# Kernel optimization log

Measured on AMD Instinct MI355X. Metric: run time of the kernel, lower is better.

Reference implementation:

```python
import jax, jax.numpy as jnp
import numpy as np

H = 128; ED = 16; NF = 200000; EI = 800000; NT = 20000; M = 4; NM = NT * M; EG = 320000; NHEADS = 4


def _ln(x, g, b):
    mu = x.mean(-1, keepdims=True)
    v = ((x - mu) ** 2).mean(-1, keepdims=True)
    return (x - mu) / jnp.sqrt(v + 1e-5) * g + b


def _bn(x, g, b):
    mu = x.mean(0)
    v = ((x - mu) ** 2).mean(0)
    return (x - mu) / jnp.sqrt(v + 1e-5) * g + b


def _gine(x, ei, ea, We, be, W1, b1, W2, b2):
    # GINEConv: msg = relu(x_j + Lin(e_ji)), sum-aggr, eps=0, 2-layer MLP
    msg = jax.nn.relu(x[ei[0]] + ea @ We.T + be)
    agg = jax.ops.segment_sum(msg, ei[1], num_segments=x.shape[0])
    z = x + agg
    return jax.nn.relu(z @ W1.T + b1) @ W2.T + b2


def _view_attn(x, ln1_g, ln1_b, ln2_g, ln2_b, Wqkv, bqkv, Wo, bo, fW1, fb1, fW2, fb2):
    N, m, Hd = x.shape
    dh = Hd // NHEADS
    r = _ln(x, ln1_g, ln1_b)
    qkv = r @ Wqkv.T + bqkv
    q, k, v = jnp.split(qkv, 3, axis=-1)
    q = q.reshape(N, m, NHEADS, dh)
    k = k.reshape(N, m, NHEADS, dh)
    v = v.reshape(N, m, NHEADS, dh)
    s = jnp.einsum('nqhd,nkhd->nhqk', q, k) * (dh ** -0.5)
    a = jax.nn.softmax(s, axis=-1)
    o = jnp.einsum('nhqk,nkhd->nqhd', a, v).reshape(N, m, Hd)
    x = x + o @ Wo.T + bo
    y = _ln(x, ln2_g, ln2_b)
    x = x + jax.nn.gelu(y @ fW1.T + fb1, approximate=False) @ fW2.T + fb2
    return x.mean(axis=1)


def setup_inputs() -> dict:
    key = jax.random.key(0)
    ks = jax.random.split(key, 48)
    rn = lambda i, shape, s=0.02: jax.random.normal(ks[i], shape, jnp.float32) * s
    inp = {}
    inp['h_flat'] = jax.random.normal(ks[0], (NF, H), jnp.float32)
    inp['ea_flat'] = jax.random.normal(ks[1], (EI, ED), jnp.float32)
    inp['edge_attr'] = jax.random.normal(ks[2], (EG, ED), jnp.float32)
    inp['intra_ei'] = jax.random.randint(ks[3], (2, EI), 0, NF)
    inp['edge_index'] = jax.random.randint(ks[4], (2, EG), 0, NT)
    inp['node_ids'] = jax.random.randint(ks[5], (NF,), 0, NT)
    inp['sub_batch'] = jax.random.randint(ks[6], (NF,), 0, NM)
    inp['root_flat_idx'] = jax.random.randint(ks[7], (NM,), 0, NF)
    inp['valid'] = jnp.ones((NF,), jnp.bool_)
    inp['N_total'] = NT
    inp['m'] = M
    inp['Wskip'] = rn(8, (H, H)); inp['bskip'] = jnp.zeros((H,))
    inp['Wvv'] = rn(9, (H, H)); inp['bvv'] = jnp.zeros((H,))
    inp['Wkk'] = rn(10, (H, H)); inp['bkk'] = jnp.zeros((H,))
    inp['lc_We'] = rn(11, (H, ED)); inp['lc_be'] = jnp.zeros((H,))
    inp['lc_W1'] = rn(12, (H, H)); inp['lc_b1'] = jnp.zeros((H,))
    inp['lc_W2'] = rn(13, (H, H)); inp['lc_b2'] = jnp.zeros((H,))
    inp['gc_We'] = rn(14, (H, ED)); inp['gc_be'] = jnp.zeros((H,))
    inp['gc_W1'] = rn(15, (H, H)); inp['gc_b1'] = jnp.zeros((H,))
    inp['gc_W2'] = rn(16, (H, H)); inp['gc_b2'] = jnp.zeros((H,))
    inp['lbn_g'] = jnp.ones((H,)); inp['lbn_b'] = jnp.zeros((H,))
    inp['gbn_g'] = jnp.ones((H,)); inp['gbn_b'] = jnp.zeros((H,))
    inp['ln1_g'] = jnp.ones((H,)); inp['ln1_b'] = jnp.zeros((H,))
    inp['ln2_g'] = jnp.ones((H,)); inp['ln2_b'] = jnp.zeros((H,))
    inp['Wqkv'] = rn(17, (3 * H, H)); inp['bqkv'] = jnp.zeros((3 * H,))
    inp['Wo'] = rn(18, (H, H)); inp['bo'] = jnp.zeros((H,))
    inp['ffn_W1'] = rn(19, (4 * H, H)); inp['ffn_b1'] = jnp.zeros((4 * H,))
    inp['ffn_W2'] = rn(20, (H, 4 * H)); inp['ffn_b2'] = jnp.zeros((H,))
    return inp


def reference(h_flat, ea_flat, edge_attr, intra_ei, edge_index, node_ids, sub_batch,
              root_flat_idx, valid, N_total, m,
              Wskip, bskip, Wvv, bvv, Wkk, bkk,
              lc_We, lc_be, lc_W1, lc_b1, lc_W2, lc_b2,
              gc_We, gc_be, gc_W1, gc_b1, gc_W2, gc_b2,
              lbn_g, lbn_b, gbn_g, gbn_b,
              ln1_g, ln1_b, ln2_g, ln2_b,
              Wqkv, bqkv, Wo, bo, ffn_W1, ffn_b1, ffn_W2, ffn_b2):
    valid_f = valid.astype(jnp.float32)[:, None]                      # [NF,1]
    clamped = jnp.maximum(node_ids, 0)
    valid_mask = (node_ids >= 0).astype(jnp.float32)[:, None]
    h_skip = (h_flat @ Wskip.T + bskip) * valid_f
    h1 = _gine(h_flat, intra_ei, ea_flat, lc_We, lc_be, lc_W1, lc_b1, lc_W2, lc_b2)
    h1 = _bn(h1, lbn_g, lbn_b) * valid_f
    # scatter-mean of valid rows into N_total global nodes
    sums = jax.ops.segment_sum(h_flat * valid_mask, clamped, num_segments=N_total)
    cnt = jax.ops.segment_sum(valid_mask, clamped, num_segments=N_total)
    x_sum = sums / jnp.maximum(cnt, 1.0)
    h_global = _gine(x_sum, edge_index, edge_attr, gc_We, gc_be, gc_W1, gc_b1, gc_W2, gc_b2)
    h2 = _bn(h_global, gbn_g, gbn_b)[clamped] * valid_f
    h_roots3d = h_flat[root_flat_idx].reshape(N_total, m, H)
    x_vv_node = _view_attn(h_roots3d, ln1_g, ln1_b, ln2_g, ln2_b, Wqkv, bqkv, Wo, bo,
                           ffn_W1, ffn_b1, ffn_W2, ffn_b2)
    x_vv = (x_vv_node[clamped] @ Wvv.T + bvv) * valid_f
    x_kk = (h_flat[root_flat_idx[sub_batch]] @ Wkk.T + bkk) * valid_f
    out = jax.nn.relu(h_skip + h1 + h2 + x_vv + x_kk)
    return out * valid_f
```

## Files before the change

### kernel.cpp

```cpp
#include <hip/hip_runtime.h>
#include <math.h>

typedef __bf16 bf16_t;
typedef bf16_t bf16x8 __attribute__((ext_vector_type(8)));
typedef float  f32x4  __attribute__((ext_vector_type(4)));

#define DEV static __device__ __forceinline__

constexpr int H  = 128, ED = 16;
constexpr int NF = 200000, EI = 800000, NT = 20000, MV = 4, NM = NT*MV, EG = 320000;

DEV bf16x8 ldb8(const bf16_t* p){ union{uint4 u; bf16x8 v;} t; t.u = *(const uint4*)p; return t.v; }
DEV void   stb8(bf16_t* p, bf16x8 v){ union{uint4 u; bf16x8 f;} t; t.f=v; *(uint4*)p = t.u; }

DEV bf16x8 cvt8(const float* p){
  float4 a = *(const float4*)p, b = *(const float4*)(p+4);
  bf16x8 r;
  r[0]=(bf16_t)a.x; r[1]=(bf16_t)a.y; r[2]=(bf16_t)a.z; r[3]=(bf16_t)a.w;
  r[4]=(bf16_t)b.x; r[5]=(bf16_t)b.y; r[6]=(bf16_t)b.z; r[7]=(bf16_t)b.w;
  return r;
}
DEV bf16x8 cvtadd8(const float* p, const float* q){
  float4 a = *(const float4*)p, b = *(const float4*)(p+4);
  float4 c = *(const float4*)q, d = *(const float4*)(q+4);
  bf16x8 r;
  r[0]=(bf16_t)(a.x+c.x); r[1]=(bf16_t)(a.y+c.y); r[2]=(bf16_t)(a.z+c.z); r[3]=(bf16_t)(a.w+c.w);
  r[4]=(bf16_t)(b.x+d.x); r[5]=(bf16_t)(b.y+d.y); r[6]=(bf16_t)(b.z+d.z); r[7]=(bf16_t)(b.w+d.w);
  return r;
}

struct GArgs {
  const float*  A;      const bf16_t* Abf;   const float* Aadd;  const int* gidx;
  const float*  W;      const float*  bias;
  float*        outf;   bf16_t*       outb;
  const float*  Xadd_f; const bf16_t* Xadd_b; const int* gidx2;
  const bf16_t* B1;     const bf16_t* h2pre; const float* yvv;  const bf16_t* ykk;
  const int*    node_ids; const int*  sub_batch; const float* affine;
  int nrows; int ldout;
};

constexpr int A_F32=0, A_F32_ADD=1, A_BF16=2, A_F32_GATHER=3;
constexpr int E_BIAS_BF16=0, E_RELU_BF16=1, E_GELU_BF16=2, E_BIAS_F32=3,
              E_ADDGATHER_BF16=4, E_ADDROW_BF16=5, E_FINAL=6;

template<int AM>
DEV bf16x8 loadA(const GArgs& g, int row, int koff, int K){
  if constexpr (AM==A_BF16)        return ldb8(g.Abf + (size_t)row*K + koff);
  else if constexpr (AM==A_F32)    return cvt8(g.A   + (size_t)row*K + koff);
  else if constexpr (AM==A_F32_GATHER) return cvt8(g.A + (size_t)g.gidx[row]*K + koff);
  else { size_t o = (size_t)row*K + koff; return cvtadd8(g.A + o, g.Aadd + o); }
}

template<int K, int CTPW, int AM, int EPI>
__global__ __launch_bounds__(256) void k_gemm(GArgs g){
  constexpr int NS = K/32;
  const int lane = threadIdx.x & 63;
  const int wave = threadIdx.x >> 6;
  const int quad = lane >> 4;
  const int r16  = lane & 15;
  const int colBase = (blockIdx.y*4 + wave)*(CTPW*16);

  bf16x8 bfrag[CTPW][NS];
  float  bcol[CTPW];
  #pragma unroll
  for (int c=0;c<CTPW;c++){
    const float* wrow = g.W + (size_t)(colBase + c*16 + r16)*K;
    #pragma unroll
    for (int s=0;s<NS;s++) bfrag[c][s] = cvt8(wrow + s*32 + quad*8);
    bcol[c] = g.bias[colBase + c*16 + r16];
  }
  float aLc[CTPW], bLc[CTPW], aGc[CTPW], bGc[CTPW];
  if constexpr (EPI==E_FINAL){
    #pragma unroll
    for (int c=0;c<CTPW;c++){
      int col = colBase + c*16 + r16;
      aLc[c]=g.affine[col];     bLc[c]=g.affine[128+col];
      aGc[c]=g.affine[256+col]; bGc[c]=g.affine[384+col];
    }
  }

  const int row0 = blockIdx.x*64;
  #pragma unroll 1
  for (int t=0;t<4;t++){
    int rowbase = row0 + t*16;
    if (rowbase >= g.nrows) break;
    int arow = rowbase + r16;
    f32x4 acc[CTPW] = {};
    #pragma unroll
    for (int s=0;s<NS;s++){
      bf16x8 af = loadA<AM>(g, arow, s*32 + quad*8, K);
      #pragma unroll
      for (int c=0;c<CTPW;c++)
        acc[c] = __builtin_amdgcn_mfma_f32_16x16x32_bf16(af, bfrag[c][s], acc[c], 0, 0, 0);
    }
    #pragma unroll
    for (int r=0;r<4;r++){
      int orow = rowbase + quad*4 + r;
      int nid=0, sb=0, g2=0;
      if constexpr (EPI==E_FINAL){ nid = g.node_ids[orow]; sb = g.sub_batch[orow]; }
      if constexpr (EPI==E_ADDGATHER_BF16){ g2 = g.gidx2[orow]; }
      #pragma unroll
      for (int c=0;c<CTPW;c++){
        int col = colBase + c*16 + r16;
        float v = acc[c][r] + bcol[c];
        size_t oidx = (size_t)orow*g.ldout + col;
        if constexpr (EPI==E_BIAS_BF16)      g.outb[oidx] = (bf16_t)v;
        else if constexpr (EPI==E_RELU_BF16) g.outb[oidx] = (bf16_t)fmaxf(v,0.f);
        else if constexpr (EPI==E_GELU_BF16){
          float gv = 0.5f*v*(1.f + erff(v*0.70710678118654752f));
          g.outb[oidx] = (bf16_t)gv;
        }
        else if constexpr (EPI==E_BIAS_F32)  g.outf[oidx] = v;
        else if constexpr (EPI==E_ADDGATHER_BF16){
          v += g.Xadd_f[(size_t)g2*128 + col];
          g.outb[oidx] = (bf16_t)v;
        }
        else if constexpr (EPI==E_ADDROW_BF16){
          v += (float)g.Xadd_b[(size_t)orow*128 + col];
          g.outb[oidx] = (bf16_t)v;
        }
        else if constexpr (EPI==E_FINAL){
          v += (float)g.ykk[(size_t)sb*128 + col];
          v += g.yvv[(size_t)nid*128 + col];
          v += (float)g.B1[(size_t)orow*128 + col]*aLc[c] + bLc[c];
          v += (float)g.h2pre[(size_t)nid*128 + col]*aGc[c] + bGc[c];
          g.outf[oidx] = fmaxf(v, 0.f);
        }
      }
    }
  }
}

template<int CHUNK>
__global__ __launch_bounds__(256) void k_edge(const float* x, const float* ea, const int* ei,
                                              const float* We, const float* be, float* agg, int E){
  __shared__ float eaL[CHUNK*16];
  __shared__ int   srcL[CHUNK], dstL[CHUNK];
  const int c = threadIdx.x & 127, half = threadIdx.x >> 7;
  float w[16];
  #pragma unroll
  for (int d=0;d<16;d++) w[d] = We[c*16+d];
  const float bc = be[c];
  const int e0 = blockIdx.x * CHUNK;
  for (int i=threadIdx.x; i<CHUNK*16; i+=256) eaL[i] = ea[(size_t)e0*16 + i];
  for (int i=threadIdx.x; i<CHUNK;    i+=256){ srcL[i]=ei[e0+i]; dstL[i]=ei[(size_t)E+e0+i]; }
  __syncthreads();
  for (int i=half; i<CHUNK; i+=2){
    const float4* ep = (const float4*)(eaL + i*16);
    float4 e1=ep[0], e2=ep[1], e3=ep[2], e4=ep[3];
    float p = bc;
    p += e1.x*w[0] + e1.y*w[1] + e1.z*w[2] + e1.w*w[3];
    p += e2.x*w[4] + e2.y*w[5] + e2.z*w[6] + e2.w*w[7];
    p += e3.x*w[8] + e3.y*w[9] + e3.z*w[10]+ e3.w*w[11];
    p += e4.x*w[12]+ e4.y*w[13]+ e4.z*w[14]+ e4.w*w[15];
    float msg = fmaxf(x[(size_t)srcL[i]*128 + c] + p, 0.f);
    atomicAdd(agg + (size_t)dstL[i]*128 + c, msg);
  }
}

__global__ __launch_bounds__(256) void k_smean(const float* h, const int* nid, float* xs, float* cnt){
  int gid = blockIdx.x*256 + threadIdx.x;
  int i = gid >> 5;
  if (i >= NF) return;
  int q = gid & 31;
  int t = nid[i];
  float4 v = *(const float4*)(h + (size_t)i*128 + q*4);
  float* d = xs + (size_t)t*128 + q*4;
  atomicAdd(d+0, v.x); atomicAdd(d+1, v.y); atomicAdd(d+2, v.z); atomicAdd(d+3, v.w);
  if (q==0) atomicAdd(cnt + t, 1.f);
}

__global__ __launch_bounds__(256) void k_div(float* xs, const float* cnt){
  int gid = blockIdx.x*256 + threadIdx.x;
  int n = gid >> 5;
  if (n >= NT) return;
  int q = gid & 31;
  float inv = 1.f / fmaxf(cnt[n], 1.f);
  float4* p = (float4*)(xs + (size_t)n*128 + q*4);
  float4 v = *p;
  v.x*=inv; v.y*=inv; v.z*=inv; v.w*=inv;
  *p = v;
}

__global__ __launch_bounds__(256) void k_stats(const bf16_t* X, int nrows, float* stats){
  int c = threadIdx.x & 127, ro = threadIdx.x >> 7;
  int r0 = blockIdx.x*256;
  int rend = (r0+256 < nrows) ? r0+256 : nrows;
  float s1=0.f, s2=0.f;
  for (int i=r0+ro; i<rend; i+=2){
    float v = (float)X[(size_t)i*128 + c];
    s1 += v; s2 += v*v;
  }
  atomicAdd(stats + c,       s1);
  atomicAdd(stats + 128 + c, s2);
}

__global__ void k_affine(const float* sL, const float* sG,
                         const float* lg, const float* lb, const float* gg, const float* gb,
                         float nL, float nG, float* aff){
  int c = threadIdx.x;
  float muL = sL[c]/nL, vL = sL[128+c]/nL - muL*muL;
  float aL = lg[c]*rsqrtf(vL + 1e-5f);
  aff[c] = aL; aff[128+c] = lb[c] - muL*aL;
  float muG = sG[c]/nG, vG = sG[128+c]/nG - muG*muG;
  float aG = gg[c]*rsqrtf(vG + 1e-5f);
  aff[256+c] = aG; aff[384+c] = gb[c] - muG*aG;
}

template<int MODE>
__global__ __launch_bounds__(256) void k_ln(const float* Xf, const bf16_t* Xb, const int* gidx,
                                            const float* gamma, const float* beta, bf16_t* outp, int nrows){
  int wave = threadIdx.x >> 6, lane = threadIdx.x & 63;
  int row = blockIdx.x*4 + wave;
  if (row >= nrows) return;
  int c0 = lane*2;
  float x0, x1;
  if constexpr (MODE==0){
    const float* p = Xf + (size_t)gidx[row]*128;
    x0 = p[c0]; x1 = p[c0+1];
  } else {
    const bf16_t* p = Xb + (size_t)row*128;
    x0 = (float)p[c0]; x1 = (float)p[c0+1];
  }
  float s = x0 + x1, q = x0*x0 + x1*x1;
  #pragma unroll
  for (int m=1; m<64; m<<=1){ s += __shfl_xor(s, m); q += __shfl_xor(q, m); }
  float mu = s*(1.f/128.f);
  float var = q*(1.f/128.f) - mu*mu;
  float rs = rsqrtf(var + 1e-5f);
  outp[(size_t)row*128 + c0]   = (bf16_t)((x0-mu)*rs*gamma[c0]   + beta[c0]);
  outp[(size_t)row*128 + c0+1] = (bf16_t)((x1-mu)*rs*gamma[c0+1] + beta[c0+1]);
}

__global__ __launch_bounds__(256) void k_attn(const bf16_t* qkv, bf16_t* o, int nnodes){
  int wave = threadIdx.x >> 6, lane = threadIdx.x & 63;
  int node = blockIdx.x*4 + wave;
  if (node >= nnodes) return;
  int qv = lane >> 4, hh = (lane >> 2) & 3, sub = lane & 3;
  size_t base = (size_t)node*4*384;
  int coff = hh*32 + sub*8;
  bf16x8 qf = ldb8(qkv + base + (size_t)qv*384 + coff);
  float s[4];
  #pragma unroll
  for (int kv=0;kv<4;kv++){
    bf16x8 kf = ldb8(qkv + base + (size_t)kv*384 + 128 + coff);
    float p = 0.f;
    #pragma unroll
    for (int j=0;j<8;j++) p += (float)qf[j]*(float)kf[j];
    p += __shfl_xor(p, 1);
    p += __shfl_xor(p, 2);
    s[kv] = p * 0.17677669529663687f;
  }
  float mx = fmaxf(fmaxf(s[0],s[1]), fmaxf(s[2],s[3]));
  float e[4]; float sm = 0.f;
  #pragma unroll
  for (int kv=0;kv<4;kv++){ e[kv] = expf(s[kv]-mx); sm += e[kv]; }
  float inv = 1.f/sm;
  float ov[8] = {0,0,0,0,0,0,0,0};
  #pragma unroll
  for (int kv=0;kv<4;kv++){
    float a = e[kv]*inv;
    bf16x8 vf = ldb8(qkv + base + (size_t)kv*384 + 256 + coff);
    #pragma unroll
    for (int j=0;j<8;j++) ov[j] += a*(float)vf[j];
  }
  bf16x8 of;
  #pragma unroll
  for (int j=0;j<8;j++) of[j] = (bf16_t)ov[j];
  stb8(o + (size_t)(node*4+qv)*128 + coff, of);
}

__global__ __launch_bounds__(256) void k_mean(const bf16_t* z2, bf16_t* xvvn){
  int gid = blockIdx.x*256 + threadIdx.x;
  if (gid >= NT*128) return;
  int n = gid >> 7, c = gid & 127;
  size_t b = (size_t)n*4*128 + c;
  float v = (float)z2[b] + (float)z2[b+128] + (float)z2[b+256] + (float)z2[b+384];
  xvvn[(size_t)n*128 + c] = (bf16_t)(v*0.25f);
}

extern "C" void kernel_launch(void* const* d_in, const int* in_sizes, int n_in,
                              void* d_out, int out_size, void* d_ws, size_t ws_size,
                              hipStream_t stream)
{
  const float* h_flat    = (const float*)d_in[0];
  const float* ea_flat   = (const float*)d_in[1];
  const float* edge_attr = (const float*)d_in[2];
  const int*   intra_ei  = (const int*)d_in[3];
  const int*   edge_index= (const int*)d_in[4];
  const int*   node_ids  = (const int*)d_in[5];
  const int*   sub_batch = (const int*)d_in[6];
  const int*   root_idx  = (const int*)d_in[7];
  const float* Wskip = (const float*)d_in[11]; const float* bskip = (const float*)d_in[12];
  const float* Wvv   = (const float*)d_in[13]; const float* bvv   = (const float*)d_in[14];
  const float* Wkk   = (const float*)d_in[15]; const float* bkk   = (const float*)d_in[16];
  const float* lc_We = (const float*)d_in[17]; const float* lc_be = (const float*)d_in[18];
  const float* lc_W1 = (const float*)d_in[19]; const float* lc_b1 = (const float*)d_in[20];
  const float* lc_W2 = (const float*)d_in[21]; const float* lc_b2 = (const float*)d_in[22];
  const float* gc_We = (const float*)d_in[23]; const float* gc_be = (const float*)d_in[24];
  const float* gc_W1 = (const float*)d_in[25]; const float* gc_b1 = (const float*)d_in[26];
  const float* gc_W2 = (const float*)d_in[27]; const float* gc_b2 = (const float*)d_in[28];
  const float* lbn_g = (const float*)d_in[29]; const float* lbn_b = (const float*)d_in[30];
  const float* gbn_g = (const float*)d_in[31]; const float* gbn_b = (const float*)d_in[32];
  const float* ln1_g = (const float*)d_in[33]; const float* ln1_b = (const float*)d_in[34];
  const float* ln2_g = (const float*)d_in[35]; const float* ln2_b = (const float*)d_in[36];
  const float* Wqkv  = (const float*)d_in[37]; const float* bqkv  = (const float*)d_in[38];
  const float* Wo    = (const float*)d_in[39]; const float* bo    = (const float*)d_in[40];
  const float* fW1   = (const float*)d_in[41]; const float* fb1   = (const float*)d_in[42];
  const float* fW2   = (const float*)d_in[43]; const float* fb2   = (const float*)d_in[44];
  float* out = (float*)d_out;

  char* base = (char*)d_ws;
  size_t off = 0;
  auto carve = [&](size_t bytes)->char* {
    char* p = base + off; off += (bytes + 255) & ~(size_t)255; return p;
  };
  float*  agg   = (float*) carve((size_t)NF*H*4);
  bf16_t* qkv   = (bf16_t*)agg;
  bf16_t* tbuf  = (bf16_t*)carve((size_t)NM*512*2);
  bf16_t* mid   = tbuf;
  bf16_t* B1    = (bf16_t*)carve((size_t)NF*H*2);
  bf16_t* rbuf  = (bf16_t*)carve((size_t)NM*H*2);
  bf16_t* z2    = rbuf;
  bf16_t* obuf  = (bf16_t*)carve((size_t)NM*H*2);
  bf16_t* xattn = (bf16_t*)carve((size_t)NM*H*2);
  bf16_t* ykk   = xattn;
  bf16_t* ybuf  = (bf16_t*)carve((size_t)NM*H*2);
  float*  x_sum = (float*) carve((size_t)NT*H*4);
  float*  yvv   = x_sum;
  float*  aggG  = (float*) carve((size_t)NT*H*4);
  float*  cnt   = (float*) carve((size_t)NT*4);
  bf16_t* tG    = (bf16_t*)carve((size_t)NT*H*2);
  bf16_t* h2pre = (bf16_t*)carve((size_t)NT*H*2);
  bf16_t* xvvn  = (bf16_t*)carve((size_t)NT*H*2);
  float*  statsL= (float*) carve(256*4);
  float*  statsG= (float*) carve(256*4);
  float*  affine= (float*) carve(512*4);
  if (off > ws_size) return;

  hipMemsetAsync(agg,    0, (size_t)NF*H*4, stream);
  hipMemsetAsync(x_sum,  0, (size_t)NT*H*4, stream);
  hipMemsetAsync(aggG,   0, (size_t)NT*H*4, stream);
  hipMemsetAsync(cnt,    0, (size_t)NT*4,   stream);
  hipMemsetAsync(statsL, 0, 2048,           stream);

  auto GX = [](int n){ return (unsigned)((n + 63) / 64); };

  k_edge<64><<<EI/64, 256, 0, stream>>>(h_flat, ea_flat, intra_ei, lc_We, lc_be, agg, EI);
  k_smean<<<(NF*32)/256, 256, 0, stream>>>(h_flat, node_ids, x_sum, cnt);
  k_div<<<(NT*32)/256, 256, 0, stream>>>(x_sum, cnt);
  k_edge<64><<<EG/64, 256, 0, stream>>>(x_sum, edge_attr, edge_index, gc_We, gc_be, aggG, EG);
  { GArgs a{}; a.A=x_sum; a.Aadd=aggG; a.W=gc_W1; a.bias=gc_b1; a.outb=tG; a.nrows=NT; a.ldout=H;
    k_gemm<128,2,A_F32_ADD,E_RELU_BF16><<<dim3(GX(NT),1), 256, 0, stream>>>(a); }
  { GArgs a{}; a.Abf=tG; a.W=gc_W2; a.bias=gc_b2; a.outb=h2pre; a.nrows=NT; a.ldout=H;
    k_gemm<128,2,A_BF16,E_BIAS_BF16><<<dim3(GX(NT),1), 256, 0, stream>>>(a); }
  k_stats<<<(NT+255)/256, 256, 0, stream>>>(h2pre, NT, statsG);
  { GArgs a{}; a.A=h_flat; a.Aadd=agg; a.W=lc_W1; a.bias=lc_b1; a.outb=tbuf; a.nrows=NF; a.ldout=H;
    k_gemm<128,2,A_F32_ADD,E_RELU_BF16><<<dim3(GX(NF),1), 256, 0, stream>>>(a); }
  { GArgs a{}; a.Abf=tbuf; a.W=lc_W2; a.bias=lc_b2; a.outb=B1; a.nrows=NF; a.ldout=H;
    k_gemm<128,2,A_BF16,E_BIAS_BF16><<<dim3(GX(NF),1), 256, 0, stream>>>(a); }
  k_stats<<<(NF+255)/256, 256, 0, stream>>>(B1, NF, statsL);
  k_affine<<<1, 128, 0, stream>>>(statsL, statsG, lbn_g, lbn_b, gbn_g, gbn_b, (float)NF, (float)NT, affine);
  k_ln<0><<<NM/4, 256, 0, stream>>>(h_flat, nullptr, root_idx, ln1_g, ln1_b, rbuf, NM);
  { GArgs a{}; a.Abf=rbuf; a.W=Wqkv; a.bias=bqkv; a.outb=qkv; a.nrows=NM; a.ldout=384;
    k_gemm<128,2,A_BF16,E_BIAS_BF16><<<dim3(GX(NM),3), 256, 0, stream>>>(a); }
  k_attn<<<NT/4, 256, 0, stream>>>(qkv, obuf, NT);
  { GArgs a{}; a.Abf=obuf; a.W=Wo; a.bias=bo; a.Xadd_f=h_flat; a.gidx2=root_idx;
    a.outb=xattn; a.nrows=NM; a.ldout=H;
    k_gemm<128,2,A_BF16,E_ADDGATHER_BF16><<<dim3(GX(NM),1), 256, 0, stream>>>(a); }
  k_ln<1><<<NM/4, 256, 0, stream>>>(nullptr, xattn, nullptr, ln2_g, ln2_b, ybuf, NM);
  { GArgs a{}; a.Abf=ybuf; a.W=fW1; a.bias=fb1; a.outb=mid; a.nrows=NM; a.ldout=512;
    k_gemm<128,2,A_BF16,E_GELU_BF16><<<dim3(GX(NM),4), 256, 0, stream>>>(a); }
  { GArgs a{}; a.Abf=mid; a.W=fW2; a.bias=fb2; a.Xadd_b=xattn; a.outb=z2; a.nrows=NM; a.ldout=H;
    k_gemm<512,1,A_BF16,E_ADDROW_BF16><<<dim3(GX(NM),2), 256, 0, stream>>>(a); }
  k_mean<<<(NT*H)/256, 256, 0, stream>>>(z2, xvvn);
  { GArgs a{}; a.Abf=xvvn; a.W=Wvv; a.bias=bvv; a.outf=yvv; a.nrows=NT; a.ldout=H;
    k_gemm<128,2,A_BF16,E_BIAS_F32><<<dim3(GX(NT),1), 256, 0, stream>>>(a); }
  { GArgs a{}; a.A=h_flat; a.gidx=root_idx; a.W=Wkk; a.bias=bkk; a.outb=ykk; a.nrows=NM; a.ldout=H;
    k_gemm<128,2,A_F32_GATHER,E_BIAS_BF16><<<dim3(GX(NM),1), 256, 0, stream>>>(a); }
  { GArgs a{}; a.A=h_flat; a.W=Wskip; a.bias=bskip; a.outf=out; a.nrows=NF; a.ldout=H;
    a.B1=B1; a.h2pre=h2pre; a.yvv=yvv; a.ykk=ykk;
    a.node_ids=node_ids; a.sub_batch=sub_batch; a.affine=affine;
    k_gemm<128,2,A_F32,E_FINAL><<<dim3(GX(NF),1), 256, 0, stream>>>(a); }
}
```

Measured before the change: 1.892 ms.

## Replace atomic scatter aggregation with per-call CSR build and gather-based segment sums

After: 1.815 ms. 4.1% less time.

```diff
diff --git a/kernel.cpp b/kernel.cpp
--- a/kernel.cpp
+++ b/kernel.cpp
@@ -9,6 +9,15 @@
 
 constexpr int H  = 128, ED = 16;
 constexpr int NF = 200000, EI = 800000, NT = 20000, MV = 4, NM = NT*MV, EG = 320000;
+
+constexpr int NB_LOCAL = 200192;
+constexpr int NB_MEAN  = 20224;
+constexpr int NB_GLOB  = 20224;
+constexpr int MB_BASE  = NB_LOCAL;
+constexpr int GB_BASE  = NB_LOCAL + NB_MEAN;
+constexpr int NB       = NB_LOCAL + NB_MEAN + NB_GLOB;
+constexpr int NBLK     = NB / 256;
+constexpr int TOTW     = EI + NF + EG;
 
 DEV bf16x8 ldb8(const bf16_t* p){ union{uint4 u; bf16x8 v;} t; t.u = *(const uint4*)p; return t.v; }
 DEV void   stb8(bf16_t* p, bf16x8 v){ union{uint4 u; bf16x8 f;} t; t.f=v; *(uint4*)p = t.u; }
@@ -131,55 +140,118 @@
   }
 }
 
-template<int CHUNK>
-__global__ __launch_bounds__(256) void k_edge(const float* x, const float* ea, const int* ei,
-                                              const float* We, const float* be, float* agg, int E){
-  __shared__ float eaL[CHUNK*16];
-  __shared__ int   srcL[CHUNK], dstL[CHUNK];
-  const int c = threadIdx.x & 127, half = threadIdx.x >> 7;
-  float w[16];
-  #pragma unroll
-  for (int d=0;d<16;d++) w[d] = We[c*16+d];
-  const float bc = be[c];
-  const int e0 = blockIdx.x * CHUNK;
-  for (int i=threadIdx.x; i<CHUNK*16; i+=256) eaL[i] = ea[(size_t)e0*16 + i];
-  for (int i=threadIdx.x; i<CHUNK;    i+=256){ srcL[i]=ei[e0+i]; dstL[i]=ei[(size_t)E+e0+i]; }
+__global__ __launch_bounds__(256) void k_hist(const int* eil_dst, const int* nid,
+                                              const int* eig_dst, int* cnt){
+  int i = blockIdx.x*256 + threadIdx.x;
+  if (i < EI)            atomicAdd(&cnt[eil_dst[i]], 1);
+  else if (i < EI+NF)    atomicAdd(&cnt[MB_BASE + nid[i-EI]], 1);
+  else if (i < TOTW)     atomicAdd(&cnt[GB_BASE + eig_dst[i-EI-NF]], 1);
+}
+
+__global__ __launch_bounds__(256) void k_scan1(const int* cnt, int* off, int* bsum){
+  __shared__ int s[256];
+  int tid = threadIdx.x;
+  int i = blockIdx.x*256 + tid;
+  int v = cnt[i];
+  s[tid] = v; __syncthreads();
+  #pragma unroll
+  for (int d=1; d<256; d<<=1){
+    int t = (tid>=d) ? s[tid-d] : 0;
+    __syncthreads();
+    s[tid] += t;
+    __syncthreads();
+  }
+  off[i] = s[tid] - v;
+  if (tid==255) bsum[blockIdx.x] = s[255];
+}
+
+__global__ __launch_bounds__(256) void k_scan2(int* bsum){
+  __shared__ int s[NBLK];
+  for (int i=threadIdx.x; i<NBLK; i+=256) s[i]=bsum[i];
   __syncthreads();
-  for (int i=half; i<CHUNK; i+=2){
-    const float4* ep = (const float4*)(eaL + i*16);
-    float4 e1=ep[0], e2=ep[1], e3=ep[2], e4=ep[3];
-    float p = bc;
-    p += e1.x*w[0] + e1.y*w[1] + e1.z*w[2] + e1.w*w[3];
-    p += e2.x*w[4] + e2.y*w[5] + e2.z*w[6] + e2.w*w[7];
-    p += e3.x*w[8] + e3.y*w[9] + e3.z*w[10]+ e3.w*w[11];
-    p += e4.x*w[12]+ e4.y*w[13]+ e4.z*w[14]+ e4.w*w[15];
-    float msg = fmaxf(x[(size_t)srcL[i]*128 + c] + p, 0.f);
-    atomicAdd(agg + (size_t)dstL[i]*128 + c, msg);
-  }
-}
-
-__global__ __launch_bounds__(256) void k_smean(const float* h, const int* nid, float* xs, float* cnt){
-  int gid = blockIdx.x*256 + threadIdx.x;
-  int i = gid >> 5;
-  if (i >= NF) return;
-  int q = gid & 31;
-  int t = nid[i];
-  float4 v = *(const float4*)(h + (size_t)i*128 + q*4);
-  float* d = xs + (size_t)t*128 + q*4;
-  atomicAdd(d+0, v.x); atomicAdd(d+1, v.y); atomicAdd(d+2, v.z); atomicAdd(d+3, v.w);
-  if (q==0) atomicAdd(cnt + t, 1.f);
-}
-
-__global__ __launch_bounds__(256) void k_div(float* xs, const float* cnt){
-  int gid = blockIdx.x*256 + threadIdx.x;
-  int n = gid >> 5;
+  if (threadIdx.x==0){
+    int run = 0;
+    for (int b=0;b<NBLK;b++){
+      if (b == NB_LOCAL/256 || b == GB_BASE/256) run = 0;
+      int v = s[b]; s[b] = run; run += v;
+    }
+  }
+  __syncthreads();
+  for (int i=threadIdx.x; i<NBLK; i+=256) bsum[i]=s[i];
+}
+
+__global__ __launch_bounds__(256) void k_scan3(int* off, const int* bsum, int* cur){
+  int i = blockIdx.x*256 + threadIdx.x;
+  int v = off[i] + bsum[blockIdx.x];
+  off[i] = v; cur[i] = v;
+}
+
+__global__ __launch_bounds__(256) void k_fill(const int* eil_dst, const int* nid,
+                                              const int* eig_dst, int* cur, int* eidx){
+  int i = blockIdx.x*256 + threadIdx.x;
+  if (i < EI){
+    int p = atomicAdd(&cur[eil_dst[i]], 1);
+    eidx[p] = i;
+  } else if (i < EI+NF){
+    int j = i - EI;
+    int p = atomicAdd(&cur[MB_BASE + nid[j]], 1);
+    eidx[EI + p] = j;
+  } else if (i < TOTW){
+    int j = i - EI - NF;
+    int p = atomicAdd(&cur[GB_BASE + eig_dst[j]], 1);
+    eidx[EI + NF + p] = j;
+  }
+}
+
+__global__ __launch_bounds__(256) void k_gmean(const float* h, const int* off, const int* eidx,
+                                               float* xs){
+  int wave = threadIdx.x >> 6, lane = threadIdx.x & 63;
+  int n = blockIdx.x*4 + wave;
   if (n >= NT) return;
-  int q = gid & 31;
-  float inv = 1.f / fmaxf(cnt[n], 1.f);
-  float4* p = (float4*)(xs + (size_t)n*128 + q*4);
-  float4 v = *p;
-  v.x*=inv; v.y*=inv; v.z*=inv; v.w*=inv;
-  *p = v;
+  int o0 = off[MB_BASE + n], o1 = off[MB_BASE + n + 1];
+  int c0 = lane*2;
+  float ax=0.f, ay=0.f;
+  for (int p=o0; p<o1; ++p){
+    int r = eidx[EI + p];
+    float2 v = *(const float2*)(h + (size_t)r*128 + c0);
+    ax += v.x; ay += v.y;
+  }
+  float inv = 1.f / fmaxf((float)(o1-o0), 1.f);
+  float2 o; o.x = ax*inv; o.y = ay*inv;
+  *(float2*)(xs + (size_t)n*128 + c0) = o;
+}
+
+__global__ __launch_bounds__(256) void k_agg(const float* x, const float* ea, const int* ei_src,
+                                             const int* off, const int* eidx,
+                                             const float* We, const float* be,
+                                             float* agg, int binBase, int eBase, int nrows){
+  int wave = threadIdx.x >> 6, lane = threadIdx.x & 63;
+  int c0 = lane*2;
+  float w0[16], w1[16];
+  #pragma unroll
+  for (int j=0;j<16;j++){ w0[j] = We[c0*16+j]; w1[j] = We[(c0+1)*16+j]; }
+  const float b0 = be[c0], b1 = be[c0+1];
+  const int stride = gridDim.x*4;
+  for (int r = blockIdx.x*4 + wave; r < nrows; r += stride){
+    int o0 = off[binBase + r], o1 = off[binBase + r + 1];
+    float ax=0.f, ay=0.f;
+    for (int p=o0; p<o1; ++p){
+      int e   = eidx[eBase + p];
+      int src = ei_src[e];
+      float val = ea[(size_t)e*16 + (lane & 15)];
+      float d0 = b0, d1 = b1;
+      #pragma unroll
+      for (int j=0;j<16;j++){
+        float a = __shfl(val, j);
+        d0 += a*w0[j]; d1 += a*w1[j];
+      }
+      float2 xs = *(const float2*)(x + (size_t)src*128 + c0);
+      ax += fmaxf(xs.x + d0, 0.f);
+      ay += fmaxf(xs.y + d1, 0.f);
+    }
+    float2 o; o.x = ax; o.y = ay;
+    *(float2*)(agg + (size_t)r*128 + c0) = o;
+  }
 }
 
 __global__ __launch_bounds__(256) void k_stats(const bf16_t* X, int nrows, float* stats){
@@ -310,10 +382,13 @@
   const float* fW2   = (const float*)d_in[43]; const float* fb2   = (const float*)d_in[44];
   float* out = (float*)d_out;
 
+  const int* eil_dst = intra_ei + EI;
+  const int* eig_dst = edge_index + EG;
+
   char* base = (char*)d_ws;
-  size_t off = 0;
+  size_t off_b = 0;
   auto carve = [&](size_t bytes)->char* {
-    char* p = base + off; off += (bytes + 255) & ~(size_t)255; return p;
+    char* p = base + off_b; off_b += (bytes + 255) & ~(size_t)255; return p;
   };
   float*  agg   = (float*) carve((size_t)NF*H*4);
   bf16_t* qkv   = (bf16_t*)agg;
@@ -329,27 +404,38 @@
   float*  x_sum = (float*) carve((size_t)NT*H*4);
   float*  yvv   = x_sum;
   float*  aggG  = (float*) carve((size_t)NT*H*4);
-  float*  cnt   = (float*) carve((size_t)NT*4);
   bf16_t* tG    = (bf16_t*)carve((size_t)NT*H*2);
   bf16_t* h2pre = (bf16_t*)carve((size_t)NT*H*2);
   bf16_t* xvvn  = (bf16_t*)carve((size_t)NT*H*2);
   float*  statsL= (float*) carve(256*4);
   float*  statsG= (float*) carve(256*4);
   float*  affine= (float*) carve(512*4);
-  if (off > ws_size) return;
-
-  hipMemsetAsync(agg,    0, (size_t)NF*H*4, stream);
-  hipMemsetAsync(x_sum,  0, (size_t)NT*H*4, stream);
-  hipMemsetAsync(aggG,   0, (size_t)NT*H*4, stream);
-  hipMemsetAsync(cnt,    0, (size_t)NT*4,   stream);
-  hipMemsetAsync(statsL, 0, 2048,           stream);
+  if (off_b > ws_size) return;
+
+  int* csr      = (int*)tbuf;
+  int* cnt_bins = csr;
+  int* offs     = cnt_bins + NB;
+  int* cur      = offs + NB;
+  int* bsum     = cur + NB;
+  int* eidx     = bsum + ((NBLK+63)&~63);
+
+  hipMemsetAsync(cnt_bins, 0, (size_t)NB*4, stream);
+  hipMemsetAsync(statsL,   0, 2048,         stream);
 
   auto GX = [](int n){ return (unsigned)((n + 63) / 64); };
 
-  k_edge<64><<<EI/64, 256, 0, stream>>>(h_flat, ea_flat, intra_ei, lc_We, lc_be, agg, EI);
-  k_smean<<<(NF*32)/256, 256, 0, stream>>>(h_flat, node_ids, x_sum, cnt);
-  k_div<<<(NT*32)/256, 256, 0, stream>>>(x_sum, cnt);
-  k_edge<64><<<EG/64, 256, 0, stream>>>(x_sum, edge_attr, edge_index, gc_We, gc_be, aggG, EG);
+  k_hist <<<(TOTW+255)/256, 256, 0, stream>>>(eil_dst, node_ids, eig_dst, cnt_bins);
+  k_scan1<<<NBLK, 256, 0, stream>>>(cnt_bins, offs, bsum);
+  k_scan2<<<1,    256, 0, stream>>>(bsum);
+  k_scan3<<<NBLK, 256, 0, stream>>>(offs, bsum, cur);
+  k_fill <<<(TOTW+255)/256, 256, 0, stream>>>(eil_dst, node_ids, eig_dst, cur, eidx);
+
+  k_gmean<<<NT/4, 256, 0, stream>>>(h_flat, offs, eidx, x_sum);
+  k_agg  <<<3125, 256, 0, stream>>>(h_flat, ea_flat,   intra_ei,   offs, eidx, lc_We, lc_be,
+                                    agg,  0,       0,     NF);
+  k_agg  <<<313,  256, 0, stream>>>(x_sum,  edge_attr, edge_index, offs, eidx, gc_We, gc_be,
+                                    aggG, GB_BASE, EI+NF, NT);
+
   { GArgs a{}; a.A=x_sum; a.Aadd=aggG; a.W=gc_W1; a.bias=gc_b1; a.outb=tG; a.nrows=NT; a.ldout=H;
     k_gemm<128,2,A_F32_ADD,E_RELU_BF16><<<dim3(GX(NT),1), 256, 0, stream>>>(a); }
   { GArgs a{}; a.Abf=tG; a.W=gc_W2; a.bias=gc_b2; a.outb=h2pre; a.nrows=NT; a.ldout=H;
```
